# Optimization experiments

Hardware: AMD Instinct MI355X
Metric: run time of the kernel (lower is better)

The kernel has to match this reference:

```python
import jax, jax.numpy as jnp
import numpy as np

B, SX, SL, D, H = 4, 4096, 256, 1024, 16
DH = D // H
LN_EPS = 1e-5
RMS_EPS = 1e-8


def layernorm(x, g, b):
    mu = jnp.mean(x, axis=-1, keepdims=True)
    var = jnp.mean(jnp.square(x - mu), axis=-1, keepdims=True)
    return (x - mu) * jax.lax.rsqrt(var + LN_EPS) * g + b


def rmsnorm(x, gamma):
    # torch: norm = ||x||_2 * dim^-0.5 ; x / clamp(norm, eps) * gamma
    norm = jnp.sqrt(jnp.sum(jnp.square(x), axis=-1, keepdims=True)) * (DH ** -0.5)
    return x / jnp.maximum(norm, RMS_EPS) * gamma


def setup_inputs() -> dict:
    key = jax.random.key(0)
    ks = jax.random.split(key, 6)
    s = 0.02
    return {
        "x": jax.random.normal(ks[0], (B, SX, D), jnp.float32),
        "latents": jax.random.normal(ks[1], (B, SL, D), jnp.float32),
        "mask_x": jnp.ones((B, SX), jnp.float32),
        "mask_latent": jnp.ones((B, SL), jnp.float32),
        "ln_x_g": jnp.ones((D,), jnp.float32),
        "ln_x_b": jnp.zeros((D,), jnp.float32),
        "ln_l_g": jnp.ones((D,), jnp.float32),
        "ln_l_b": jnp.zeros((D,), jnp.float32),
        "Wq": jax.random.normal(ks[2], (D, D), jnp.float32) * s,
        "Wkv": jax.random.normal(ks[3], (D, 2 * D), jnp.float32) * s,
        "qk_gamma": jnp.ones((DH,), jnp.float32),
        "Wo": jax.random.normal(ks[4], (D, D), jnp.float32) * s,
    }


def reference(x, latents, mask_x, mask_latent, ln_x_g, ln_x_b, ln_l_g, ln_l_b, Wq, Wkv, qk_gamma, Wo):
    xn = layernorm(x, ln_x_g, ln_x_b)                       # [B,SX,D]
    ln = layernorm(latents, ln_l_g, ln_l_b)                 # [B,SL,D]

    q = (ln @ Wq).reshape(B, SL, H, DH).transpose(0, 2, 1, 3)      # [B,H,SL,DH]
    kv_in = jnp.concatenate([xn, ln], axis=1)                      # [B,SX+SL,D]
    kv = kv_in @ Wkv
    Skv = SX + SL
    k = kv[..., :D].reshape(B, Skv, H, DH).transpose(0, 2, 1, 3)   # [B,H,Skv,DH]
    v = kv[..., D:].reshape(B, Skv, H, DH).transpose(0, 2, 1, 3)

    # NOTE: original code applies query_norm to BOTH q and k (faithful to source)
    q = rmsnorm(q, qk_gamma)
    k = rmsnorm(k, qk_gamma)

    scores = jnp.einsum("bhqd,bhkd->bhqk", q, k) / np.sqrt(DH)     # [B,H,SL,Skv]

    kv_mask = jnp.concatenate([mask_x, mask_latent], axis=1)       # [B,Skv]
    mask = kv_mask[:, None, :] * mask_latent[:, :, None]           # [B,SL,Skv]
    add_mask = (1.0 - mask)[:, None, :, :] * jnp.finfo(scores.dtype).min
    attn = jax.nn.softmax(scores + add_mask, axis=-1)

    y = jnp.einsum("bhqk,bhkd->bhqd", attn, v)                     # [B,H,SL,DH]
    y = y.transpose(0, 2, 1, 3).reshape(B, SL, D)
    return y @ Wo
```

## Files before the change

### kernel.cpp

```cpp
#include <hip/hip_runtime.h>

#define NB   4
#define SXX  4096
#define SLL  256
#define DD   1024
#define HH   16
#define DHH  64
#define SKV  4352
#define MKV  17408
#define NSPLIT 8

typedef __attribute__((ext_vector_type(8))) short bfrag;
typedef __attribute__((ext_vector_type(4))) float facc;

__device__ __forceinline__ unsigned short f2bf(float f){
  unsigned u = __builtin_bit_cast(unsigned, f);
  u = (u + 0x7fffu + ((u >> 16) & 1u)) >> 16;
  return (unsigned short)u;
}
__device__ __forceinline__ float bf2f(unsigned short h){
  unsigned u = ((unsigned)h) << 16;
  return __builtin_bit_cast(float, u);
}

#define GLOAD_LDS16(g, lds) __builtin_amdgcn_global_load_lds( \
    (const __attribute__((address_space(1))) unsigned int*)(const void*)(g), \
    (__attribute__((address_space(3))) unsigned int*)(void*)(lds), 16, 0, 0)

__global__ void wtrans3(const float* __restrict__ Wq, const float* __restrict__ Wkv,
                        const float* __restrict__ Wo, unsigned short* __restrict__ wqt,
                        unsigned short* __restrict__ wkvt, unsigned short* __restrict__ wot){
  __shared__ float t[32][33];
  int z = blockIdx.z;
  const float* in; unsigned short* out; int N;
  if (z == 0){ in = Wq;  out = wqt;  N = DD;   }
  else if (z == 1){ in = Wkv; out = wkvt; N = 2*DD; }
  else { in = Wo;  out = wot;  N = DD;   }
  int n0 = blockIdx.x * 32, k0 = blockIdx.y * 32;
  if (n0 >= N) return;
  int tx = threadIdx.x, ty = threadIdx.y;
  #pragma unroll
  for (int i = 0; i < 4; i++)
    t[ty + 8*i][tx] = in[(size_t)(k0 + ty + 8*i) * N + n0 + tx];
  __syncthreads();
  #pragma unroll
  for (int i = 0; i < 4; i++)
    out[(size_t)(n0 + ty + 8*i) * DD + k0 + tx] = f2bf(t[tx][ty + 8*i]);
}

__global__ __launch_bounds__(256) void lnorm2(const float* __restrict__ x,
    const float* __restrict__ lat,
    const float* __restrict__ gx, const float* __restrict__ bx,
    const float* __restrict__ gl, const float* __restrict__ bl,
    unsigned short* __restrict__ kvin, unsigned short* __restrict__ lnlat){
  int t = threadIdx.x, w = t >> 6, l = t & 63;
  int gr = blockIdx.x * 4 + w;
  const float* src; const float* g; const float* bt;
  unsigned short* d2 = nullptr;
  int b, s, off;
  if (gr < NB*SXX){
    b = gr >> 12; s = gr & 4095; off = 0;
    src = x + (size_t)gr * DD; g = gx; bt = bx;
  } else {
    int r = gr - NB*SXX;
    b = r >> 8; s = r & 255; off = SXX;
    src = lat + (size_t)r * DD; g = gl; bt = bl;
    d2 = lnlat + (size_t)r * DD;
  }
  const float4* rp = (const float4*)src;
  float4 v[4];
  float sum = 0.f, sq = 0.f;
  #pragma unroll
  for (int i = 0; i < 4; i++){
    v[i] = rp[l + i*64];
    sum += v[i].x + v[i].y + v[i].z + v[i].w;
    sq  += v[i].x*v[i].x + v[i].y*v[i].y + v[i].z*v[i].z + v[i].w*v[i].w;
  }
  #pragma unroll
  for (int o = 1; o < 64; o <<= 1){ sum += __shfl_xor(sum, o); sq += __shfl_xor(sq, o); }
  float mu = sum * (1.f/DD);
  float rs = rsqrtf(sq*(1.f/DD) - mu*mu + 1e-5f);
  unsigned short* dst = kvin + (size_t)(b*SKV + off + s) * DD;
  #pragma unroll
  for (int i = 0; i < 4; i++){
    float4 gv = ((const float4*)g)[l + i*64];
    float4 bv = ((const float4*)bt)[l + i*64];
    ushort4 o4;
    o4.x = f2bf((v[i].x - mu)*rs*gv.x + bv.x);
    o4.y = f2bf((v[i].y - mu)*rs*gv.y + bv.y);
    o4.z = f2bf((v[i].z - mu)*rs*gv.z + bv.z);
    o4.w = f2bf((v[i].w - mu)*rs*gv.w + bv.w);
    *(ushort4*)(dst + (size_t)(l + i*64)*4) = o4;
    if (d2) *(ushort4*)(d2 + (size_t)(l + i*64)*4) = o4;
  }
}

__global__ __launch_bounds__(256) void gemm64(const unsigned short* __restrict__ A,
    const unsigned short* __restrict__ Bt, int M, int N, int K, float* __restrict__ outF){
  __shared__ alignas(16) unsigned short lA[64*64];
  __shared__ alignas(16) unsigned short lB[64*64];
  int n0 = blockIdx.x * 64, m0 = blockIdx.y * 64;
  int t = threadIdx.x, w = t >> 6, l = t & 63;
  int wr = (w >> 1) * 32, wc = (w & 1) * 32;
  int lr = l & 15, q2 = l >> 4;
  int rA = w*8 + (l >> 3), u = l & 7;
  int swz = (u ^ (rA & 7)) * 8;
  const unsigned short* Ag = A  + (size_t)(m0 + rA) * K + swz;
  const unsigned short* Bg = Bt + (size_t)(n0 + rA) * K + swz;
  facc acc00 = (facc)0.f, acc01 = (facc)0.f, acc10 = (facc)0.f, acc11 = (facc)0.f;
  for (int k0 = 0; k0 < K; k0 += 64){
    GLOAD_LDS16(Ag + k0,                 &lA[(w*8)*64]);
    GLOAD_LDS16(Ag + (size_t)32*K + k0,  &lA[(32 + w*8)*64]);
    GLOAD_LDS16(Bg + k0,                 &lB[(w*8)*64]);
    GLOAD_LDS16(Bg + (size_t)32*K + k0,  &lB[(32 + w*8)*64]);
    __syncthreads();
    #pragma unroll
    for (int ks = 0; ks < 2; ks++){
      int cs = ((ks*4 + q2) ^ (lr & 7)) * 8;
      bfrag a0 = *(const bfrag*)&lA[(wr + lr)*64 + cs];
      bfrag a1 = *(const bfrag*)&lA[(wr + 16 + lr)*64 + cs];
      bfrag b0 = *(const bfrag*)&lB[(wc + lr)*64 + cs];
      bfrag b1 = *(const bfrag*)&lB[(wc + 16 + lr)*64 + cs];
      acc00 = __builtin_amdgcn_mfma_f32_16x16x32_bf16(a0, b0, acc00, 0, 0, 0);
      acc01 = __builtin_amdgcn_mfma_f32_16x16x32_bf16(a0, b1, acc01, 0, 0, 0);
      acc10 = __builtin_amdgcn_mfma_f32_16x16x32_bf16(a1, b0, acc10, 0, 0, 0);
      acc11 = __builtin_amdgcn_mfma_f32_16x16x32_bf16(a1, b1, acc11, 0, 0, 0);
    }
    __syncthreads();
  }
  int rl = (l >> 4) * 4, cl = l & 15;
  facc accs[2][2] = {{acc00, acc01},{acc10, acc11}};
  #pragma unroll
  for (int mt = 0; mt < 2; mt++)
  #pragma unroll
  for (int nt = 0; nt < 2; nt++)
  #pragma unroll
  for (int j = 0; j < 4; j++){
    int r = m0 + wr + mt*16 + rl + j;
    int c = n0 + wc + nt*16 + cl;
    outF[(size_t)r * N + c] = accs[mt][nt][j];
  }
}

__global__ __launch_bounds__(256) void gemm_q(const unsigned short* __restrict__ A,
    const unsigned short* __restrict__ Bt, const float* __restrict__ gamma,
    unsigned short* __restrict__ qn){
  __shared__ alignas(16) char smemb[18432];
  unsigned short* lA = (unsigned short*)smemb;
  unsigned short* lB = lA + 64*64;
  float* Cf = (float*)smemb;
  int h = blockIdx.x, n0 = h * 64, m0 = blockIdx.y * 64;
  int t = threadIdx.x, w = t >> 6, l = t & 63;
  int wr = (w >> 1) * 32, wc = (w & 1) * 32;
  int lr = l & 15, q2 = l >> 4;
  int rA = w*8 + (l >> 3), u = l & 7;
  int swz = (u ^ (rA & 7)) * 8;
  const unsigned short* Ag = A  + (size_t)(m0 + rA) * 1024 + swz;
  const unsigned short* Bg = Bt + (size_t)(n0 + rA) * 1024 + swz;
  facc acc00 = (facc)0.f, acc01 = (facc)0.f, acc10 = (facc)0.f, acc11 = (facc)0.f;
  for (int k0 = 0; k0 < 1024; k0 += 64){
    GLOAD_LDS16(Ag + k0,          &lA[(w*8)*64]);
    GLOAD_LDS16(Ag + 32768 + k0,  &lA[(32 + w*8)*64]);
    GLOAD_LDS16(Bg + k0,          &lB[(w*8)*64]);
    GLOAD_LDS16(Bg + 32768 + k0,  &lB[(32 + w*8)*64]);
    __syncthreads();
    #pragma unroll
    for (int ks = 0; ks < 2; ks++){
      int cs = ((ks*4 + q2) ^ (lr & 7)) * 8;
      bfrag a0 = *(const bfrag*)&lA[(wr + lr)*64 + cs];
      bfrag a1 = *(const bfrag*)&lA[(wr + 16 + lr)*64 + cs];
      bfrag b0 = *(const bfrag*)&lB[(wc + lr)*64 + cs];
      bfrag b1 = *(const bfrag*)&lB[(wc + 16 + lr)*64 + cs];
      acc00 = __builtin_amdgcn_mfma_f32_16x16x32_bf16(a0, b0, acc00, 0, 0, 0);
      acc01 = __builtin_amdgcn_mfma_f32_16x16x32_bf16(a0, b1, acc01, 0, 0, 0);
      acc10 = __builtin_amdgcn_mfma_f32_16x16x32_bf16(a1, b0, acc10, 0, 0, 0);
      acc11 = __builtin_amdgcn_mfma_f32_16x16x32_bf16(a1, b1, acc11, 0, 0, 0);
    }
    __syncthreads();
  }
  int rl = (l >> 4) * 4, cl = l & 15;
  facc accs[2][2] = {{acc00, acc01},{acc10, acc11}};
  #pragma unroll
  for (int mt = 0; mt < 2; mt++)
  #pragma unroll
  for (int nt = 0; nt < 2; nt++)
  #pragma unroll
  for (int j = 0; j < 4; j++)
    Cf[(wr + mt*16 + rl + j)*66 + wc + nt*16 + cl] = accs[mt][nt][j];
  __syncthreads();
  if (t < 64){
    const float* src = &Cf[t*66];
    float ss = 0.f;
    #pragma unroll
    for (int d = 0; d < 64; d++){ float a = src[d]; ss = fmaf(a, a, ss); }
    float rv = 0.125f / fmaxf(sqrtf(ss) * 0.125f, 1e-8f);
    int r = m0 + t, b = r >> 8, sl = r & 255;
    unsigned short* dst = &qn[((size_t)(b*HH + h)*SLL + sl)*DHH];
    #pragma unroll
    for (int i = 0; i < 8; i++){
      ushort4 p; float g;
      g = gamma[i*8+0]; p.x = f2bf(src[i*8+0]*g*g*rv);
      g = gamma[i*8+1]; p.y = f2bf(src[i*8+1]*g*g*rv);
      g = gamma[i*8+2]; p.z = f2bf(src[i*8+2]*g*g*rv);
      g = gamma[i*8+3]; p.w = f2bf(src[i*8+3]*g*g*rv);
      ushort4 q;
      g = gamma[i*8+4]; q.x = f2bf(src[i*8+4]*g*g*rv);
      g = gamma[i*8+5]; q.y = f2bf(src[i*8+5]*g*g*rv);
      g = gamma[i*8+6]; q.z = f2bf(src[i*8+6]*g*g*rv);
      g = gamma[i*8+7]; q.w = f2bf(src[i*8+7]*g*g*rv);
      *(ushort4*)&dst[i*8]     = p;
      *(ushort4*)&dst[i*8 + 4] = q;
    }
  }
}

__global__ __launch_bounds__(512, 2) void gemm_kv(const unsigned short* __restrict__ A,
    const unsigned short* __restrict__ Bt,
    const float* __restrict__ mask_x, const float* __restrict__ mask_lat,
    unsigned short* __restrict__ outK, unsigned short* __restrict__ outV,
    float* __restrict__ rkm){
  __shared__ alignas(16) unsigned short lds[3 * 24576];
  int bid = blockIdx.x;
  int wg = (bid & 7) * 136 + (bid >> 3);
  int m0 = (wg >> 4) * 256, n0 = (wg & 15) * 128;
  int t = threadIdx.x, w = t >> 6, l = t & 63;
  int wm = w >> 1, wn = w & 1;
  int lr = l & 15, q2 = l >> 4;
  int r8 = l >> 3, u = l & 7;
  int swz = (u ^ (r8 & 7)) * 8;
  const unsigned short* Ag = A  + (size_t)(m0 + w*8 + r8) * 1024 + swz;
  const unsigned short* Bg = Bt + (size_t)(n0 + w*8 + r8) * 1024 + swz;

  facc acc[4][4];
  #pragma unroll
  for (int mt = 0; mt < 4; mt++)
  #pragma unroll
  for (int nt = 0; nt < 4; nt++) acc[mt][nt] = (facc)0.f;

#define SBAR __builtin_amdgcn_sched_barrier(0)
#define KV_BARRIER do { SBAR; __builtin_amdgcn_s_barrier(); SBAR; } while(0)
#define KV_STA(j, i) GLOAD_LDS16(Ag + (size_t)(i)*65536 + (j)*64, \
    &lds[((j) % 3)*24576 + (i)*4096 + w*512])
#define KV_STB(j, i) GLOAD_LDS16(Bg + (size_t)(i)*65536 + (j)*64, \
    &lds[((j) % 3)*24576 + 16384 + (i)*4096 + w*512])
#define KV_LDF(va, vb, j, ks) { \
    const unsigned short* pA = &lds[((j) % 3)*24576 + (wm*64 + lr)*64 + (((ks)*4 + q2) ^ (lr & 7))*8]; \
    const unsigned short* pB = &lds[((j) % 3)*24576 + 16384 + (wn*64 + lr)*64 + (((ks)*4 + q2) ^ (lr & 7))*8]; \
    va[0] = *(const bfrag*)(pA);        va[1] = *(const bfrag*)(pA + 1024); \
    va[2] = *(const bfrag*)(pA + 2048); va[3] = *(const bfrag*)(pA + 3072); \
    vb[0] = *(const bfrag*)(pB);        vb[1] = *(const bfrag*)(pB + 1024); \
    vb[2] = *(const bfrag*)(pB + 2048); vb[3] = *(const bfrag*)(pB + 3072); }
#define KV_MFMA(va, vb) do { \
    __builtin_amdgcn_s_setprio(1); \
    _Pragma("unroll") \
    for (int mt = 0; mt < 4; mt++){ \
      _Pragma("unroll") \
      for (int nt = 0; nt < 4; nt++) \
        acc[mt][nt] = __builtin_amdgcn_mfma_f32_16x16x32_bf16(va[mt], vb[nt], acc[mt][nt], 0, 0, 0); } \
    __builtin_amdgcn_s_setprio(0); } while(0)

  KV_STA(0,0); KV_STA(0,1); KV_STA(0,2); KV_STA(0,3); KV_STB(0,0); KV_STB(0,1);
  KV_STA(1,0); KV_STA(1,1); KV_STA(1,2); KV_STA(1,3); KV_STB(1,0); KV_STB(1,1);
  __asm__ volatile("s_waitcnt vmcnt(6)" ::: "memory");
  KV_BARRIER;

  bfrag av[4], bv[4];
  #pragma unroll
  for (int j = 0; j < 16; j++){
    KV_LDF(av, bv, j, 0);
    if (j < 14){ KV_STA(j+2, 0); KV_STA(j+2, 1); KV_STB(j+2, 0); }
    KV_MFMA(av, bv);
    KV_LDF(av, bv, j, 1);
    if (j < 14){ KV_STA(j+2, 2); KV_STA(j+2, 3); KV_STB(j+2, 1); }
    KV_MFMA(av, bv);
    if (j < 14)       { __asm__ volatile("s_waitcnt vmcnt(6)" ::: "memory"); }
    else if (j == 14) { __asm__ volatile("s_waitcnt vmcnt(0)" ::: "memory"); }
    KV_BARRIER;
  }
#undef KV_STA
#undef KV_STB
#undef KV_LDF
#undef KV_MFMA

  int b = m0 / SKV, s0 = m0 - b*SKV;
  if (n0 < DD){
    #pragma unroll
    for (int mt = 0; mt < 4; mt++)
    #pragma unroll
    for (int nt = 0; nt < 4; nt++)
    #pragma unroll
    for (int j = 0; j < 4; j++)
      lds[(wm*64 + mt*16 + q2*4 + j)*136 + wn*64 + nt*16 + lr] = f2bf(acc[mt][nt][j]);
    __syncthreads();
    int s = t >> 1, hf = t & 1;
    int srow = s0 + s;
    float cm = (srow < SXX) ? mask_x[b*SXX + srow] : mask_lat[b*SLL + srow - SXX];
    const unsigned short* src = &lds[s*136 + hf*64];
    uint4 wv[8];
    #pragma unroll
    for (int i = 0; i < 8; i++) wv[i] = *(const uint4*)&src[i*8];
    float ss0 = 0.f, ss1 = 0.f;
    #pragma unroll
    for (int i = 0; i < 8; i++){
      const unsigned short* pp = (const unsigned short*)&wv[i];
      #pragma unroll
      for (int e = 0; e < 4; e++){
        float a = bf2f(pp[e]);     ss0 = fmaf(a, a, ss0);
        float c = bf2f(pp[e + 4]); ss1 = fmaf(c, c, ss1);
      }
    }
    float rv = 1.f / fmaxf(sqrtf(ss0 + ss1) * 0.125f, 1e-8f);
    int h = (n0 >> 6) + hf;
    unsigned short* dst = &outK[((size_t)(b*HH + h)*SKV + srow)*DHH];
    #pragma unroll
    for (int i = 0; i < 8; i++)
      *(uint4*)&dst[i*8] = wv[i];
    rkm[((size_t)(b*HH + h))*SKV + srow] = (cm != 0.f) ? rv : -1.f;
  } else {
    #pragma unroll
    for (int mt = 0; mt < 4; mt++)
    #pragma unroll
    for (int nt = 0; nt < 4; nt++){
      ushort4 p;
      p.x = f2bf(acc[mt][nt][0]); p.y = f2bf(acc[mt][nt][1]);
      p.z = f2bf(acc[mt][nt][2]); p.w = f2bf(acc[mt][nt][3]);
      *(ushort4*)&lds[(wn*64 + nt*16 + lr)*264 + wm*64 + mt*16 + q2*4] = p;
    }
    __syncthreads();
    int c = t >> 2, sq = t & 3;
    int hh = ((n0 - DD) >> 6) + (c >> 6), d = c & 63;
    const unsigned short* src = &lds[c*264 + sq*64];
    unsigned short* dst = &outV[((size_t)(b*HH + hh)*DHH + d)*SKV + s0 + sq*64];
    #pragma unroll
    for (int i = 0; i < 8; i++)
      *(uint4*)&dst[i*8] = *(const uint4*)&src[i*8];
  }
}

__global__ __launch_bounds__(256) void attn(const unsigned short* __restrict__ qn,
    const unsigned short* __restrict__ kbuf, const unsigned short* __restrict__ vT,
    const float* __restrict__ rkm, const float* __restrict__ mask_lat,
    float* __restrict__ Opart, float* __restrict__ lpart){
  int bh = blockIdx.y, split = blockIdx.z;
  int b = bh >> 4;
  __shared__ unsigned short lP[4][4][16][68];
  int t = threadIdx.x, w = t >> 6, l = t & 63;
  int lr = l & 15, q2 = l >> 4, kq = q2 * 8;
  bfrag aq0[4], aq1[4];
  float rm[4][4];
  #pragma unroll
  for (int tt = 0; tt < 4; tt++){
    const unsigned short* qbase = qn + ((size_t)bh * SLL + tt*64 + w*16 + lr) * DHH;
    aq0[tt] = *(const bfrag*)&qbase[kq];
    aq1[tt] = *(const bfrag*)&qbase[32 + kq];
    #pragma unroll
    for (int j = 0; j < 4; j++) rm[tt][j] = mask_lat[b*SLL + tt*64 + w*16 + q2*4 + j];
  }
  facc O[4][4];
  #pragma unroll
  for (int tt = 0; tt < 4; tt++)
  #pragma unroll
  for (int nt = 0; nt < 4; nt++) O[tt][nt] = (facc)0.f;
  float lsum[4][4];
  #pragma unroll
  for (int tt = 0; tt < 4; tt++)
  #pragma unroll
  for (int j = 0; j < 4; j++) lsum[tt][j] = 0.f;

  int t0 = (split * 68) / NSPLIT, t1 = ((split + 1) * 68) / NSPLIT;
  for (int kt = t0; kt < t1; kt++){
    int key0 = kt * 64;
    const unsigned short* kb = kbuf + ((size_t)bh * SKV + key0) * DHH;
    bfrag bk0[4], bk1[4]; float rk[4];
    #pragma unroll
    for (int nt = 0; nt < 4; nt++){
      bk0[nt] = *(const bfrag*)&kb[(nt*16 + lr)*DHH + kq];
      bk1[nt] = *(const bfrag*)&kb[(nt*16 + lr)*DHH + 32 + kq];
      rk[nt]  = rkm[(size_t)bh*SKV + key0 + nt*16 + lr];
    }
    const unsigned short* vb = vT + (size_t)bh * DHH * SKV + key0;
    bfrag bv0[4], bv1[4];
    #pragma unroll
    for (int nt = 0; nt < 4; nt++){
      bv0[nt] = *(const bfrag*)&vb[(size_t)(nt*16 + lr)*SKV + kq];
      bv1[nt] = *(const bfrag*)&vb[(size_t)(nt*16 + lr)*SKV + 32 + kq];
    }
    #pragma unroll
    for (int tt = 0; tt < 4; tt++){
      facc S[4];
      #pragma unroll
      for (int nt = 0; nt < 4; nt++){
        S[nt] = (facc)0.f;
        S[nt] = __builtin_amdgcn_mfma_f32_16x16x32_bf16(aq0[tt], bk0[nt], S[nt], 0, 0, 0);
        S[nt] = __builtin_amdgcn_mfma_f32_16x16x32_bf16(aq1[tt], bk1[nt], S[nt], 0, 0, 0);
      }
      #pragma unroll
      for (int j = 0; j < 4; j++){
        float rs_ = 0.f;
        #pragma unroll
        for (int nt = 0; nt < 4; nt++){
          float x = S[nt][j] * rk[nt];
          float sv = (rk[nt] >= 0.f && rm[tt][j] != 0.f) ? x : -3.0e38f;
          float p = __expf(sv - 8.0f);
          rs_ += p;
          lP[w][tt][q2*4 + j][nt*16 + lr] = f2bf(p);
        }
        lsum[tt][j] += rs_;
      }
    }
    __asm__ volatile("s_waitcnt lgkmcnt(0)" ::: "memory");
    #pragma unroll
    for (int tt = 0; tt < 4; tt++){
      bfrag ap0 = *(const bfrag*)&lP[w][tt][lr][kq];
      bfrag ap1 = *(const bfrag*)&lP[w][tt][lr][32 + kq];
      #pragma unroll
      for (int nt = 0; nt < 4; nt++){
        O[tt][nt] = __builtin_amdgcn_mfma_f32_16x16x32_bf16(ap0, bv0[nt], O[tt][nt], 0, 0, 0);
        O[tt][nt] = __builtin_amdgcn_mfma_f32_16x16x32_bf16(ap1, bv1[nt], O[tt][nt], 0, 0, 0);
      }
    }
  }
  #pragma unroll
  for (int tt = 0; tt < 4; tt++)
  #pragma unroll
  for (int j = 0; j < 4; j++){
    float L = lsum[tt][j];
    L += __shfl_xor(L, 1); L += __shfl_xor(L, 2);
    L += __shfl_xor(L, 4); L += __shfl_xor(L, 8);
    int srow = tt*64 + w*16 + q2*4 + j;
    size_t obase = (((size_t)split*64 + bh)*SLL + srow)*DHH;
    #pragma unroll
    for (int nt = 0; nt < 4; nt++)
      Opart[obase + nt*16 + lr] = O[tt][nt][j];
    if (lr == 0)
      lpart[((size_t)split*64 + bh)*SLL + srow] = L;
  }
}

__global__ __launch_bounds__(256) void attn_combine(const float* __restrict__ Opart,
    const float* __restrict__ lpart, unsigned short* __restrict__ ybuf){
  int t = threadIdx.x, w = t >> 6, l = t & 63;
  int idx = blockIdx.x * 4 + w;
  int bh = idx >> 8, srow = idx & 255;
  int b = bh >> 4, h = bh & 15;
  float L = 0.f, acc = 0.f;
  #pragma unroll
  for (int s = 0; s < NSPLIT; s++){
    L   += lpart[((size_t)s*64 + bh)*SLL + srow];
    acc += Opart[(((size_t)s*64 + bh)*SLL + srow)*DHH + l];
  }
  ybuf[((size_t)b*SLL + srow)*DD + h*DHH + l] = f2bf(acc / L);
}

extern "C" void kernel_launch(void* const* d_in, const int* in_sizes, int n_in,
                              void* d_out, int out_size, void* d_ws, size_t ws_size,
                              hipStream_t stream) {
  const float* x        = (const float*)d_in[0];
  const float* latents  = (const float*)d_in[1];
  const float* mask_x   = (const float*)d_in[2];
  const float* mask_lat = (const float*)d_in[3];
  const float* ln_x_g   = (const float*)d_in[4];
  const float* ln_x_b   = (const float*)d_in[5];
  const float* ln_l_g   = (const float*)d_in[6];
  const float* ln_l_b   = (const float*)d_in[7];
  const float* Wq       = (const float*)d_in[8];
  const float* Wkv      = (const float*)d_in[9];
  const float* qk_gamma = (const float*)d_in[10];
  const float* Wo       = (const float*)d_in[11];
  float* out = (float*)d_out;

  char* wsb = (char*)d_ws;
  unsigned short* kvin  = (unsigned short*)(wsb + 0);
  unsigned short* lnlat = (unsigned short*)(wsb + 35651584);
  unsigned short* wqt   = (unsigned short*)(wsb + 37748736);
  unsigned short* wkvt  = (unsigned short*)(wsb + 39845888);
  unsigned short* wot   = (unsigned short*)(wsb + 44040192);
  unsigned short* qnb   = (unsigned short*)(wsb + 50331648);
  unsigned short* kbuf  = (unsigned short*)(wsb + 52428800);
  unsigned short* vT    = (unsigned short*)(wsb + 88080384);
  float*          rkm   = (float*)(wsb + 123731968);
  unsigned short* ybuf  = (unsigned short*)(wsb + 124846080);
  float*          Opart = (float*)(wsb + 0);
  float*          lpart = (float*)(wsb + 35651584);

  wtrans3<<<dim3(64, 32, 3), dim3(32, 8), 0, stream>>>(Wq, Wkv, Wo, wqt, wkvt, wot);

  lnorm2<<<(NB*SXX + NB*SLL)/4, 256, 0, stream>>>(x, latents, ln_x_g, ln_x_b,
                                                  ln_l_g, ln_l_b, kvin, lnlat);

  gemm_q<<<dim3(16, 16), 256, 0, stream>>>(lnlat, wqt, qk_gamma, qnb);
  gemm_kv<<<dim3(1088), 512, 0, stream>>>(kvin, wkvt, mask_x, mask_lat, kbuf, vT, rkm);

  attn<<<dim3(1, NB*HH, NSPLIT), 256, 0, stream>>>(qnb, kbuf, vT, rkm, mask_lat, Opart, lpart);
  attn_combine<<<(NB*HH*SLL)/4, 256, 0, stream>>>(Opart, lpart, ybuf);

  gemm64<<<dim3(DD/64, (NB*SLL)/64), 256, 0, stream>>>(ybuf, wot, NB*SLL, DD, DD, out);
}
```

Before: 336.0 us.

## Double-buffer K/V tiles in LDS with async global-to-LDS loads in attention

New measurement: 318.3 us. 5.3% less time.

```diff
diff --git a/kernel.cpp b/kernel.cpp
--- a/kernel.cpp
+++ b/kernel.cpp
@@ -343,9 +343,18 @@
     float* __restrict__ Opart, float* __restrict__ lpart){
   int bh = blockIdx.y, split = blockIdx.z;
   int b = bh >> 4;
+  __shared__ alignas(16) unsigned short lK[2][4096];
+  __shared__ alignas(16) unsigned short lV[2][4096];
   __shared__ unsigned short lP[4][4][16][68];
   int t = threadIdx.x, w = t >> 6, l = t & 63;
   int lr = l & 15, q2 = l >> 4, kq = q2 * 8;
+  int r8 = l >> 3, u = l & 7;
+  int swz8 = (u ^ (r8 & 7)) * 8;
+  int cs0 = (q2 ^ (lr & 7)) * 8;
+  int cs1 = ((4 + q2) ^ (lr & 7)) * 8;
+  const unsigned short* Kg = kbuf + ((size_t)bh*SKV + w*8 + r8)*DHH + swz8;
+  const unsigned short* Vg = vT + (size_t)bh*DHH*SKV + (size_t)(w*8 + r8)*SKV + swz8;
+
   bfrag aq0[4], aq1[4];
   float rm[4][4];
   #pragma unroll
@@ -368,22 +377,36 @@
   for (int j = 0; j < 4; j++) lsum[tt][j] = 0.f;
 
   int t0 = (split * 68) / NSPLIT, t1 = ((split + 1) * 68) / NSPLIT;
+  {
+    int key0 = t0 * 64;
+    GLOAD_LDS16(Kg + (size_t)key0*DHH,          &lK[0][(w*8)*64]);
+    GLOAD_LDS16(Kg + (size_t)(key0+32)*DHH,     &lK[0][(w*8 + 32)*64]);
+    GLOAD_LDS16(Vg + key0,                      &lV[0][(w*8)*64]);
+    GLOAD_LDS16(Vg + (size_t)32*SKV + key0,     &lV[0][(w*8 + 32)*64]);
+  }
+  __asm__ volatile("s_waitcnt vmcnt(0)" ::: "memory");
+  __builtin_amdgcn_s_barrier();
+
+  int p = 0;
   for (int kt = t0; kt < t1; kt++){
     int key0 = kt * 64;
-    const unsigned short* kb = kbuf + ((size_t)bh * SKV + key0) * DHH;
-    bfrag bk0[4], bk1[4]; float rk[4];
+    bfrag bk0[4], bk1[4], bv0[4], bv1[4]; float rk[4];
     #pragma unroll
     for (int nt = 0; nt < 4; nt++){
-      bk0[nt] = *(const bfrag*)&kb[(nt*16 + lr)*DHH + kq];
-      bk1[nt] = *(const bfrag*)&kb[(nt*16 + lr)*DHH + 32 + kq];
+      const unsigned short* kr = &lK[p][(nt*16 + lr)*64];
+      const unsigned short* vr = &lV[p][(nt*16 + lr)*64];
+      bk0[nt] = *(const bfrag*)&kr[cs0];
+      bk1[nt] = *(const bfrag*)&kr[cs1];
+      bv0[nt] = *(const bfrag*)&vr[cs0];
+      bv1[nt] = *(const bfrag*)&vr[cs1];
       rk[nt]  = rkm[(size_t)bh*SKV + key0 + nt*16 + lr];
     }
-    const unsigned short* vb = vT + (size_t)bh * DHH * SKV + key0;
-    bfrag bv0[4], bv1[4];
-    #pragma unroll
-    for (int nt = 0; nt < 4; nt++){
-      bv0[nt] = *(const bfrag*)&vb[(size_t)(nt*16 + lr)*SKV + kq];
-      bv1[nt] = *(const bfrag*)&vb[(size_t)(nt*16 + lr)*SKV + 32 + kq];
+    if (kt + 1 < t1){
+      int kn = key0 + 64;
+      GLOAD_LDS16(Kg + (size_t)kn*DHH,        &lK[p^1][(w*8)*64]);
+      GLOAD_LDS16(Kg + (size_t)(kn+32)*DHH,   &lK[p^1][(w*8 + 32)*64]);
+      GLOAD_LDS16(Vg + kn,                    &lV[p^1][(w*8)*64]);
+      GLOAD_LDS16(Vg + (size_t)32*SKV + kn,   &lV[p^1][(w*8 + 32)*64]);
     }
     #pragma unroll
     for (int tt = 0; tt < 4; tt++){
@@ -401,9 +424,9 @@
         for (int nt = 0; nt < 4; nt++){
           float x = S[nt][j] * rk[nt];
           float sv = (rk[nt] >= 0.f && rm[tt][j] != 0.f) ? x : -3.0e38f;
-          float p = __expf(sv - 8.0f);
-          rs_ += p;
-          lP[w][tt][q2*4 + j][nt*16 + lr] = f2bf(p);
+          float pz = __expf(sv - 8.0f);
+          rs_ += pz;
+          lP[w][tt][q2*4 + j][nt*16 + lr] = f2bf(pz);
         }
         lsum[tt][j] += rs_;
       }
@@ -419,6 +442,9 @@
         O[tt][nt] = __builtin_amdgcn_mfma_f32_16x16x32_bf16(ap1, bv1[nt], O[tt][nt], 0, 0, 0);
       }
     }
+    __asm__ volatile("s_waitcnt vmcnt(0)" ::: "memory");
+    __builtin_amdgcn_s_barrier();
+    p ^= 1;
   }
   #pragma unroll
   for (int tt = 0; tt < 4; tt++)
```
